# Optimization experiments

Hardware: AMD Instinct MI355X
Metric: run time of the kernel (lower is better)

The kernel has to match this reference:

```python
import jax, jax.numpy as jnp
import numpy as np

H = 32        # num heads
D = 80        # head dim
HID = 2560    # hidden size = H*D
ROT = 32      # rotary dim = int(0.4*80)
THETA = 10000.0
T = 2048      # total packed tokens
B = 4         # sequences
SEQ = 512     # tokens per sequence
CACHE = 4096  # paged cache slots


def setup_inputs() -> dict:
    key = jax.random.key(0)
    ks = jax.random.split(key, 10)
    bound = 1.0 / np.sqrt(HID)

    def lin(k):
        kw, kb = jax.random.split(k)
        W = jax.random.uniform(kw, (HID, HID), jnp.float32, -bound, bound)
        b = jax.random.uniform(kb, (HID,), jnp.float32, -bound, bound)
        return W, b

    Wq, bq = lin(ks[0])
    Wk, bk = lin(ks[1])
    Wv, bv = lin(ks[2])
    Wd, bd = lin(ks[3])
    h = jax.random.normal(ks[4], (T, HID), jnp.float32)
    return {
        "h": h,
        "k_cache": jnp.zeros((CACHE, HID), jnp.float32),
        "v_cache": jnp.zeros((CACHE, HID), jnp.float32),
        "positions": (jnp.arange(T) % SEQ).astype(jnp.int32),
        "offsets": (jnp.arange(B + 1) * SEQ).astype(jnp.int32),
        "cache_indices": jnp.arange(T, dtype=jnp.int32),
        "Wq": Wq, "bq": bq, "Wk": Wk, "bk": bk,
        "Wv": Wv, "bv": bv, "Wd": Wd, "bd": bd,
    }


def _rotate_half(x):
    x1, x2 = jnp.split(x, 2, axis=-1)
    return jnp.concatenate([-x2, x1], axis=-1)


def reference(h, k_cache, v_cache, positions, offsets, cache_indices,
              Wq, bq, Wk, bk, Wv, bv, Wd, bd):
    # QKV projections (torch Linear: x @ W.T + b)
    q = h @ Wq.T + bq
    k = h @ Wk.T + bk
    v = h @ Wv.T + bv

    q3 = q.reshape(T, H, D)
    k3 = k.reshape(T, H, D)

    # partial RoPE on first ROT dims of each head
    pos = positions.astype(jnp.float32)
    inv_freq = 1.0 / (THETA ** (jnp.arange(0, ROT, 2, dtype=jnp.float32) / ROT))
    freqs = pos[:, None] * inv_freq                      # [T, ROT/2]
    emb = jnp.concatenate([freqs, freqs], axis=-1)       # [T, ROT]
    cos = jnp.cos(emb)[:, None, :]                       # [T, 1, ROT]
    sin = jnp.sin(emb)[:, None, :]

    q_rot, q_pass = q3[..., :ROT], q3[..., ROT:]
    k_rot, k_pass = k3[..., :ROT], k3[..., ROT:]
    q_rot = q_rot * cos + _rotate_half(q_rot) * sin
    k_rot = k_rot * cos + _rotate_half(k_rot) * sin
    q3 = jnp.concatenate([q_rot, q_pass], axis=-1)
    k3 = jnp.concatenate([k_rot, k_pass], axis=-1)

    # prompt_init=True path: scatter rotated k and v into paged caches
    new_k_cache = k_cache.at[cache_indices].set(k3.reshape(T, HID))
    new_v_cache = v_cache.at[cache_indices].set(v)

    # variable-length causal attention over packed sequences
    scale = D ** -0.5
    scores = jnp.einsum('thd,shd->hts', q3, k3) * scale   # [H, T, T]
    idx = jnp.arange(T)
    seg = jnp.searchsorted(offsets[1:], idx, side='right')
    mask = (seg[:, None] == seg[None, :]) & (idx[:, None] >= idx[None, :])
    scores = jnp.where(mask[None], scores, jnp.float32(-1e30))
    p = jax.nn.softmax(scores, axis=-1)
    o = jnp.einsum('hts,shd->thd', p, v.reshape(T, H, D)).reshape(T, HID)

    out = o @ Wd.T + bd
    return out, new_k_cache, new_v_cache
```

## Files before the change

### kernel.cpp

```cpp
#include <hip/hip_runtime.h>
#include <cstdint>
#include <cstddef>


#define HIDDEN 2560
#define SEQT 2048
#define NHEADS 32
#define DHEAD 80
#define NSEG 4
#define SEGLEN 512
#define CACHE_ROWS 4096
#define QSCALE 0.11180339887498949f

typedef __bf16 bf16_8 __attribute__((ext_vector_type(8)));
typedef unsigned short u16x8 __attribute__((ext_vector_type(8)));
typedef float f32x4 __attribute__((ext_vector_type(4)));

__device__ __forceinline__ unsigned short f2bf(float f) {
  unsigned int u = __builtin_bit_cast(unsigned int, f);
  u += 0x7fffu + ((u >> 16) & 1u);
  return (unsigned short)(u >> 16);
}
__device__ __forceinline__ float bf2f(unsigned short s) {
  unsigned int u = ((unsigned int)s) << 16;
  return __builtin_bit_cast(float, u);
}

__device__ __forceinline__ void gload16(const unsigned short* g, unsigned short* l) {
  __builtin_amdgcn_global_load_lds(
      (const __attribute__((address_space(1))) unsigned int*)g,
      (__attribute__((address_space(3))) unsigned int*)l, 16, 0, 0);
}

#define BAR() asm volatile("s_barrier" ::: "memory")
#define LGKM0()                                          \
  do {                                                   \
    asm volatile("s_waitcnt lgkmcnt(0)" ::: "memory");   \
    __builtin_amdgcn_sched_barrier(0);                   \
  } while (0)
#define PRIO(x) __builtin_amdgcn_s_setprio(x)
#define MF(af, bf, c) c = __builtin_amdgcn_mfma_f32_16x16x32_bf16(af, bf, c, 0, 0, 0)

__global__ __launch_bounds__(256) void cast_kernel(
    const float* __restrict__ src, unsigned short* __restrict__ dst, int n4) {
  int i = blockIdx.x * blockDim.x + threadIdx.x;
  const int stride = gridDim.x * blockDim.x;
  for (; i < n4; i += stride) {
    float4 v = ((const float4*)src)[i];
    ushort4 o;
    o.x = f2bf(v.x); o.y = f2bf(v.y); o.z = f2bf(v.z); o.w = f2bf(v.w);
    ((ushort4*)dst)[i] = o;
  }
}

__global__ __launch_bounds__(256) void cast4_kernel(
    const float* __restrict__ s0, const float* __restrict__ s1,
    const float* __restrict__ s2, const float* __restrict__ s3,
    unsigned short* __restrict__ d0, unsigned short* __restrict__ d1,
    unsigned short* __restrict__ d2, unsigned short* __restrict__ d3, int n4) {
  const float* s = blockIdx.z == 0 ? s0 : blockIdx.z == 1 ? s1 : blockIdx.z == 2 ? s2 : s3;
  unsigned short* d = blockIdx.z == 0 ? d0 : blockIdx.z == 1 ? d1 : blockIdx.z == 2 ? d2 : d3;
  int i = blockIdx.x * blockDim.x + threadIdx.x;
  const int stride = gridDim.x * blockDim.x;
  for (; i < n4; i += stride) {
    float4 v = ((const float4*)s)[i];
    ushort4 o;
    o.x = f2bf(v.x); o.y = f2bf(v.y); o.z = f2bf(v.z); o.w = f2bf(v.w);
    ((ushort4*)d)[i] = o;
  }
}

template <int OUTMODE, int NT>
__device__ __forceinline__ void gemm256_body(
    const unsigned short* __restrict__ A, const unsigned short* __restrict__ Bg,
    const float* __restrict__ bias, void* __restrict__ C,
    int m0, int n0, int kbase) {
  constexpr int K = HIDDEN;
  static_assert((NT & 1) == 0 && NT >= 4, "NT must be even");
  __shared__ __align__(16) unsigned short L[65536];

  const int tid = threadIdx.x;
  const int lane = tid & 63;
  const int wid = tid >> 6;
  const int l15 = lane & 15;
  const int kg = lane >> 4;
  const int wm = wid >> 2;
  const int wn = wid & 3;

  const int g8 = (((tid & 7) - (tid >> 3)) & 7) * 8;
  const int srow = tid >> 3;
  const unsigned short* As0 = A + (size_t)(m0 + srow) * K + kbase + g8;
  const unsigned short* As1 = As0 + (size_t)128 * K;
  const unsigned short* Bs0 = Bg + (size_t)(n0 + srow) * K + kbase + g8;
  const unsigned short* Bs1 = Bs0 + (size_t)128 * K;
  const int t16 = tid * 8;

  auto stA0 = [&](int kt) {
    const int b = (kt & 1) * 32768, ko = kt * 64;
    gload16(As0 + ko, L + b + t16);
    gload16(As1 + ko, L + b + 8192 + t16);
  };
  auto stA1 = [&](int kt) {
    const int b = (kt & 1) * 32768, ko = 64 * K + kt * 64;
    gload16(As0 + ko, L + b + 4096 + t16);
    gload16(As1 + ko, L + b + 12288 + t16);
  };
  auto stB0 = [&](int kt) {
    const int b = (kt & 1) * 32768 + 16384, ko = kt * 64;
    gload16(Bs0 + ko, L + b + t16);
    gload16(Bs0 + 64 * K + ko, L + b + 4096 + t16);
  };
  auto stB1 = [&](int kt) {
    const int b = (kt & 1) * 32768 + 16384 + 8192, ko = kt * 64;
    gload16(Bs1 + ko, L + b + t16);
    gload16(Bs1 + 64 * K + ko, L + b + 4096 + t16);
  };

  const int c0 = (kg + l15) & 7;
  const int aof0 = wm * 8192 + l15 * 64 + c0 * 8;
  const int aof1 = wm * 8192 + l15 * 64 + (c0 ^ 4) * 8;
  const int bof0 = 16384 + wn * 4096 + l15 * 64 + c0 * 8;
  const int bof1 = 16384 + wn * 4096 + l15 * 64 + (c0 ^ 4) * 8;

  f32x4 acc[8][4];
#pragma unroll
  for (int m = 0; m < 8; m++)
#pragma unroll
    for (int n = 0; n < 4; n++) acc[m][n] = f32x4{0.f, 0.f, 0.f, 0.f};

  bf16_8 a[4][2], bl[2][2], bh[2][2];

#define DSR(off) (*(const bf16_8*)(L + (off)))
  auto rdA = [&](int off) {
#pragma unroll
    for (int fm = 0; fm < 4; fm++) {
      a[fm][0] = DSR(off + aof0 + fm * 1024);
      a[fm][1] = DSR(off + aof1 + fm * 1024);
    }
  };
  auto rdBl = [&](int off) {
#pragma unroll
    for (int fn = 0; fn < 2; fn++) {
      bl[fn][0] = DSR(off + bof0 + fn * 1024);
      bl[fn][1] = DSR(off + bof1 + fn * 1024);
    }
  };
  auto rdBh = [&](int off) {
#pragma unroll
    for (int fn = 0; fn < 2; fn++) {
      bh[fn][0] = DSR(off + bof0 + (2 + fn) * 1024);
      bh[fn][1] = DSR(off + bof1 + (2 + fn) * 1024);
    }
  };
  auto mmq = [&](int mq, int nq, bf16_8 (&bb)[2][2]) {
#pragma unroll
    for (int fm = 0; fm < 4; fm++)
#pragma unroll
      for (int fn = 0; fn < 2; fn++) {
        MF(a[fm][0], bb[fn][0], acc[mq * 4 + fm][nq * 2 + fn]);
        MF(a[fm][1], bb[fn][1], acc[mq * 4 + fm][nq * 2 + fn]);
      }
  };

  stA0(0); stB0(0); stB1(0); stA1(0);
  stA0(1); stB0(1); stB1(1);
  asm volatile("s_waitcnt vmcnt(6)" ::: "memory");
  BAR();

#pragma unroll 2
  for (int t = 0; t < NT - 2; ++t) {
    const int bo = (t & 1) * 32768;
    rdA(bo); rdBl(bo);
    stA1(t + 1);
    BAR(); LGKM0(); PRIO(1); mmq(0, 0, bl); PRIO(0); BAR();
    rdBh(bo);
    stA0(t + 2);
    BAR(); LGKM0(); PRIO(1); mmq(0, 1, bh); PRIO(0); BAR();
    rdA(bo + 4096);
    stB0(t + 2);
    BAR(); LGKM0(); PRIO(1); mmq(1, 0, bl); PRIO(0); BAR();
    stB1(t + 2);
    BAR(); PRIO(1); mmq(1, 1, bh); PRIO(0);
    asm volatile("s_waitcnt vmcnt(6)" ::: "memory");
    BAR();
  }

  {
    const int bo = 0;
    rdA(bo); rdBl(bo);
    stA1(NT - 1);
    BAR(); LGKM0(); PRIO(1); mmq(0, 0, bl); PRIO(0); BAR();
    rdBh(bo);
    BAR(); LGKM0(); PRIO(1); mmq(0, 1, bh); PRIO(0); BAR();
    rdA(bo + 4096);
    BAR(); LGKM0(); PRIO(1); mmq(1, 0, bl); PRIO(0); BAR();
    BAR(); PRIO(1); mmq(1, 1, bh); PRIO(0);
    asm volatile("s_waitcnt vmcnt(0)" ::: "memory");
    BAR();
  }
  {
    const int bo = 32768;
    rdA(bo); rdBl(bo);
    BAR(); LGKM0(); PRIO(1); mmq(0, 0, bl); PRIO(0); BAR();
    rdBh(bo);
    BAR(); LGKM0(); PRIO(1); mmq(0, 1, bh); PRIO(0); BAR();
    rdA(bo + 4096);
    BAR(); LGKM0(); PRIO(1); mmq(1, 0, bl); PRIO(0); BAR();
    PRIO(1); mmq(1, 1, bh); PRIO(0);
  }
#undef DSR

#pragma unroll
  for (int n4 = 0; n4 < 4; n4++) {
    const int col = n0 + wn * 64 + n4 * 16 + l15;
    const float bv = (OUTMODE == 2) ? 0.f : bias[col];
#pragma unroll
    for (int m8 = 0; m8 < 8; m8++) {
      const int rowb = m0 + wm * 128 + m8 * 16 + kg * 4;
#pragma unroll
      for (int j = 0; j < 4; j++) {
        float val = acc[m8][n4][j] + bv;
        if (OUTMODE == 0)
          ((unsigned short*)C)[(size_t)(rowb + j) * HIDDEN + col] = f2bf(val);
        else
          ((float*)C)[(size_t)(rowb + j) * HIDDEN + col] = val;
      }
    }
  }
}

__global__ __launch_bounds__(512, 2) void gemm_qkv8_kernel(
    const unsigned short* __restrict__ A,
    const unsigned short* __restrict__ B0, const unsigned short* __restrict__ B1,
    const unsigned short* __restrict__ B2,
    const float* __restrict__ bias0, const float* __restrict__ bias1,
    const float* __restrict__ bias2,
    unsigned short* __restrict__ C0, unsigned short* __restrict__ C1,
    unsigned short* __restrict__ C2) {
  const int lb = blockIdx.x + 8 * (blockIdx.y + 10 * blockIdx.z);
  const int swz = (lb & 7) * 30 + (lb >> 3);
  const int mx = swz & 7;
  const int r = swz >> 3;
  const int ny = r % 10;
  const int zz = r / 10;
  const unsigned short* B = zz == 0 ? B0 : (zz == 1 ? B1 : B2);
  const float* bias = zz == 0 ? bias0 : (zz == 1 ? bias1 : bias2);
  unsigned short* C = zz == 0 ? C0 : (zz == 1 ? C1 : C2);
  gemm256_body<0, 40>(A, B, bias, C, mx * 256, ny * 256, 0);
}

__global__ __launch_bounds__(512, 2) void gemm_out8_kernel(
    const unsigned short* __restrict__ A, const unsigned short* __restrict__ B,
    float* __restrict__ P0, float* __restrict__ P1) {
  const int lb = blockIdx.x + 8 * (blockIdx.y + 10 * blockIdx.z);
  const int swz = (lb & 7) * 20 + (lb >> 3);
  const int mx = swz & 7;
  const int r = swz >> 3;
  const int ny = r % 10;
  const int kz = r / 10;
  float* P = kz == 0 ? P0 : P1;
  gemm256_body<2, 20>(A, B, nullptr, P, mx * 256, ny * 256, kz * 1280);
}

__global__ __launch_bounds__(256) void reduce_bias_kernel(
    const float* __restrict__ p0, const float* __restrict__ p1,
    const float* __restrict__ bias, float* __restrict__ out, int n4) {
  int i = blockIdx.x * blockDim.x + threadIdx.x;
  const int stride = gridDim.x * blockDim.x;
  for (; i < n4; i += stride) {
    float4 a = ((const float4*)p0)[i];
    float4 b = ((const float4*)p1)[i];
    const int cb = (i * 4) % HIDDEN;
    float4 bv = *(const float4*)&bias[cb];
    float4 o;
    o.x = a.x + b.x + bv.x;
    o.y = a.y + b.y + bv.y;
    o.z = a.z + b.z + bv.z;
    o.w = a.w + b.w + bv.w;
    ((float4*)out)[i] = o;
  }
}

__global__ __launch_bounds__(256) void rope_scatter_kernel(
    unsigned short* __restrict__ qb, unsigned short* __restrict__ kb,
    const unsigned short* __restrict__ vb,
    const int* __restrict__ positions, const int* __restrict__ cidx,
    float* __restrict__ kco, float* __restrict__ vco) {
  const int t = blockIdx.x;
  const int tid = threadIdx.x;
  __shared__ float cs[16], sn[16];

  if (tid < 16) {
    const float pos = (float)positions[t];
    const float inv = expf(-(float)tid * (9.210340371976184f / 16.0f));
    const float f = pos * inv;
    cs[tid] = cosf(f);
    sn[tid] = sinf(f);
  }
  __syncthreads();

  for (int i = tid; i < 1024; i += 256) {
    const int which = i >> 9;
    const int p = i & 511;
    const int hh = p >> 4, d = p & 15;
    unsigned short* buf = which ? kb : qb;
    const size_t base = (size_t)t * HIDDEN + hh * DHEAD + d;
    const float x1 = bf2f(buf[base]);
    const float x2 = bf2f(buf[base + 16]);
    const float c = cs[d], s = sn[d];
    buf[base] = f2bf(x1 * c - x2 * s);
    buf[base + 16] = f2bf(x2 * c + x1 * s);
  }
  __syncthreads();

  const int ci = cidx[t];
  float* krow = kco + (size_t)ci * HIDDEN;
  float* vrow = vco + (size_t)ci * HIDDEN;
  const unsigned short* ks = kb + (size_t)t * HIDDEN;
  const unsigned short* vs = vb + (size_t)t * HIDDEN;
  for (int i = tid; i < HIDDEN; i += 256) {
    krow[i] = bf2f(ks[i]);
    vrow[i] = bf2f(vs[i]);
  }
}

#define KSTR 104
#define VSTR 72
#define PSTR 72

__global__ __launch_bounds__(256) void attn_mfma_kernel(
    const unsigned short* __restrict__ qb, const unsigned short* __restrict__ kb,
    const unsigned short* __restrict__ vb, unsigned short* __restrict__ ob) {
  const int qt = blockIdx.x;
  const int h = blockIdx.y;
  const int seg = blockIdx.z;
  const int tq0 = seg * SEGLEN + qt * 64;

  __shared__ unsigned short Kt[64 * KSTR];
  __shared__ unsigned short VtT[80 * VSTR];
  __shared__ unsigned short Pw[4][16 * PSTR];

  const int tid = threadIdx.x;
  const int lane = tid & 63;
  const int w = tid >> 6;
  const int l15 = lane & 15;
  const int g = lane >> 4;

  bf16_8 qa[3];
  {
    const unsigned short* qp = qb + (size_t)(tq0 + w * 16 + l15) * HIDDEN + h * DHEAD;
#pragma unroll
    for (int c = 0; c < 3; c++) {
      u16x8 t = (u16x8)(unsigned short)0;
      const int d0 = c * 32 + g * 8;
      if (d0 < DHEAD) {
#pragma unroll
        for (int e = 0; e < 8; e++) t[e] = f2bf(bf2f(qp[d0 + e]) * QSCALE);
      }
      qa[c] = __builtin_bit_cast(bf16_8, t);
    }
  }

  float m_[4], l_[4];
#pragma unroll
  for (int j = 0; j < 4; j++) { m_[j] = -3.0e38f; l_[j] = 0.f; }
  f32x4 Oacc[5];
#pragma unroll
  for (int n = 0; n < 5; n++) Oacc[n] = f32x4{0.f, 0.f, 0.f, 0.f};

  for (int st = 0; st <= qt; ++st) {
    const int ts0 = seg * SEGLEN + st * 64;
    __syncthreads();
    for (int i = tid; i < 64 * 20; i += 256) {
      const int row = i / 20;
      const int c = i - row * 20;
      const size_t gsrc = (size_t)(ts0 + row) * HIDDEN + h * DHEAD + c * 4;
      ushort4 kv = *(const ushort4*)(kb + gsrc);
      ushort4 vv = *(const ushort4*)(vb + gsrc);
      *(ushort4*)&Kt[row * KSTR + c * 4] = kv;
      VtT[(c * 4 + 0) * VSTR + row] = vv.x;
      VtT[(c * 4 + 1) * VSTR + row] = vv.y;
      VtT[(c * 4 + 2) * VSTR + row] = vv.z;
      VtT[(c * 4 + 3) * VSTR + row] = vv.w;
    }
    __syncthreads();

    f32x4 Sacc[4];
#pragma unroll
    for (int t = 0; t < 4; t++) Sacc[t] = f32x4{0.f, 0.f, 0.f, 0.f};
#pragma unroll
    for (int c = 0; c < 3; c++) {
#pragma unroll
      for (int t = 0; t < 4; t++) {
        bf16_8 kf;
        if (c < 2 || g < 2)
          kf = *(const bf16_8*)&Kt[(t * 16 + l15) * KSTR + c * 32 + g * 8];
        else
          kf = __builtin_bit_cast(bf16_8, (u16x8)(unsigned short)0);
        Sacc[t] = __builtin_amdgcn_mfma_f32_16x16x32_bf16(qa[c], kf, Sacc[t], 0, 0, 0);
      }
    }

    if (st == qt) {
#pragma unroll
      for (int t = 0; t < 4; t++)
#pragma unroll
        for (int j = 0; j < 4; j++)
          if (t * 16 + l15 > w * 16 + 4 * g + j) Sacc[t][j] = -1e30f;
    }

    float pm[4], ps[4], rold[4];
#pragma unroll
    for (int j = 0; j < 4; j++)
      pm[j] = fmaxf(fmaxf(Sacc[0][j], Sacc[1][j]), fmaxf(Sacc[2][j], Sacc[3][j]));
#pragma unroll
    for (int d = 1; d < 16; d <<= 1)
#pragma unroll
      for (int j = 0; j < 4; j++) pm[j] = fmaxf(pm[j], __shfl_xor(pm[j], d, 64));
#pragma unroll
    for (int j = 0; j < 4; j++) {
      const float mn = fmaxf(m_[j], pm[j]);
      rold[j] = __expf(m_[j] - mn);
      m_[j] = mn;
      ps[j] = 0.f;
    }
#pragma unroll
    for (int t = 0; t < 4; t++)
#pragma unroll
      for (int j = 0; j < 4; j++) {
        const float p = __expf(Sacc[t][j] - m_[j]);
        Sacc[t][j] = p;
        ps[j] += p;
      }
#pragma unroll
    for (int d = 1; d < 16; d <<= 1)
#pragma unroll
      for (int j = 0; j < 4; j++) ps[j] += __shfl_xor(ps[j], d, 64);
#pragma unroll
    for (int j = 0; j < 4; j++) l_[j] = l_[j] * rold[j] + ps[j];

#pragma unroll
    for (int t = 0; t < 4; t++)
#pragma unroll
      for (int j = 0; j < 4; j++)
        Pw[w][(4 * g + j) * PSTR + t * 16 + l15] = f2bf(Sacc[t][j]);
#pragma unroll
    for (int n = 0; n < 5; n++)
#pragma unroll
      for (int j = 0; j < 4; j++) Oacc[n][j] *= rold[j];

#pragma unroll
    for (int c = 0; c < 2; c++) {
      bf16_8 pa = *(const bf16_8*)&Pw[w][l15 * PSTR + c * 32 + g * 8];
#pragma unroll
      for (int n = 0; n < 5; n++) {
        bf16_8 vf = *(const bf16_8*)&VtT[(n * 16 + l15) * VSTR + c * 32 + g * 8];
        Oacc[n] = __builtin_amdgcn_mfma_f32_16x16x32_bf16(pa, vf, Oacc[n], 0, 0, 0);
      }
    }
  }

  float inv[4];
#pragma unroll
  for (int j = 0; j < 4; j++) inv[j] = 1.f / l_[j];
  unsigned short* op = ob + (size_t)(tq0 + w * 16) * HIDDEN + h * DHEAD;
#pragma unroll
  for (int n = 0; n < 5; n++)
#pragma unroll
    for (int j = 0; j < 4; j++)
      op[(size_t)(4 * g + j) * HIDDEN + n * 16 + l15] = f2bf(Oacc[n][j] * inv[j]);
}

extern "C" void kernel_launch(void* const* d_in, const int* in_sizes, int n_in,
                              void* d_out, int out_size, void* d_ws, size_t ws_size,
                              hipStream_t stream) {
  const float* h = (const float*)d_in[0];
  const float* kci = (const float*)d_in[1];
  const float* vci = (const float*)d_in[2];
  const int* positions = (const int*)d_in[3];
  const int* cidx = (const int*)d_in[5];
  const float* Wq = (const float*)d_in[6];
  const float* bq = (const float*)d_in[7];
  const float* Wk = (const float*)d_in[8];
  const float* bk = (const float*)d_in[9];
  const float* Wv = (const float*)d_in[10];
  const float* bv = (const float*)d_in[11];
  const float* Wd = (const float*)d_in[12];
  const float* bd = (const float*)d_in[13];

  float* out = (float*)d_out;
  float* kco = out + (size_t)SEQT * HIDDEN;
  float* vco = kco + (size_t)CACHE_ROWS * HIDDEN;

  char* ws = (char*)d_ws;
  char* ws0 = ws;
  unsigned short* h_bf = (unsigned short*)ws;  ws += (size_t)SEQT * HIDDEN * 2;
  unsigned short* Wq_bf = (unsigned short*)ws; ws += (size_t)HIDDEN * HIDDEN * 2;
  unsigned short* Wk_bf = (unsigned short*)ws; ws += (size_t)HIDDEN * HIDDEN * 2;
  unsigned short* Wv_bf = (unsigned short*)ws; ws += (size_t)HIDDEN * HIDDEN * 2;
  unsigned short* Wd_bf = (unsigned short*)ws; ws += (size_t)HIDDEN * HIDDEN * 2;
  unsigned short* q_bf = (unsigned short*)ws;  ws += (size_t)SEQT * HIDDEN * 2;
  unsigned short* k_bf = (unsigned short*)ws;  ws += (size_t)SEQT * HIDDEN * 2;
  unsigned short* v_bf = (unsigned short*)ws;  ws += (size_t)SEQT * HIDDEN * 2;
  unsigned short* o_bf = (unsigned short*)ws;  ws += (size_t)SEQT * HIDDEN * 2;

  float* part0 = (float*)ws0;
  float* part1 = part0 + (size_t)SEQT * HIDDEN;

  const size_t half = (size_t)SEQT * HIDDEN;
  hipMemcpyAsync(kco + half, kci + half, half * 4, hipMemcpyDeviceToDevice, stream);
  hipMemcpyAsync(vco + half, vci + half, half * 4, hipMemcpyDeviceToDevice, stream);

  cast_kernel<<<2048, 256, 0, stream>>>(h, h_bf, SEQT * HIDDEN / 4);
  {
    dim3 gc(2048, 1, 4);
    cast4_kernel<<<gc, 256, 0, stream>>>(Wq, Wk, Wv, Wd, Wq_bf, Wk_bf, Wv_bf, Wd_bf,
                                         HIDDEN * HIDDEN / 4);
  }

  {
    dim3 gq(SEQT / 256, HIDDEN / 256, 3);
    gemm_qkv8_kernel<<<gq, 512, 0, stream>>>(h_bf, Wq_bf, Wk_bf, Wv_bf, bq, bk, bv,
                                             q_bf, k_bf, v_bf);
  }

  rope_scatter_kernel<<<SEQT, 256, 0, stream>>>(q_bf, k_bf, v_bf, positions, cidx, kco, vco);

  {
    dim3 ga(SEGLEN / 64, NHEADS, NSEG);
    attn_mfma_kernel<<<ga, 256, 0, stream>>>(q_bf, k_bf, v_bf, o_bf);
  }

  {
    dim3 go(SEQT / 256, HIDDEN / 256, 2);
    gemm_out8_kernel<<<go, 512, 0, stream>>>(o_bf, Wd_bf, part0, part1);
  }
  reduce_bias_kernel<<<2048, 256, 0, stream>>>(part0, part1, bd, out,
                                               SEQT * HIDDEN / 4);
}
```

Before: 259.4 us.

## Use three-way split-K for output GEMM and merge cast/copy launches

```diff
diff --git a/kernel.cpp b/kernel.cpp
--- a/kernel.cpp
+++ b/kernel.cpp
@@ -41,25 +41,17 @@
 #define PRIO(x) __builtin_amdgcn_s_setprio(x)
 #define MF(af, bf, c) c = __builtin_amdgcn_mfma_f32_16x16x32_bf16(af, bf, c, 0, 0, 0)
 
-__global__ __launch_bounds__(256) void cast_kernel(
-    const float* __restrict__ src, unsigned short* __restrict__ dst, int n4) {
-  int i = blockIdx.x * blockDim.x + threadIdx.x;
-  const int stride = gridDim.x * blockDim.x;
-  for (; i < n4; i += stride) {
-    float4 v = ((const float4*)src)[i];
-    ushort4 o;
-    o.x = f2bf(v.x); o.y = f2bf(v.y); o.z = f2bf(v.z); o.w = f2bf(v.w);
-    ((ushort4*)dst)[i] = o;
-  }
-}
-
-__global__ __launch_bounds__(256) void cast4_kernel(
+__global__ __launch_bounds__(256) void cast5_kernel(
     const float* __restrict__ s0, const float* __restrict__ s1,
     const float* __restrict__ s2, const float* __restrict__ s3,
+    const float* __restrict__ s4,
     unsigned short* __restrict__ d0, unsigned short* __restrict__ d1,
-    unsigned short* __restrict__ d2, unsigned short* __restrict__ d3, int n4) {
-  const float* s = blockIdx.z == 0 ? s0 : blockIdx.z == 1 ? s1 : blockIdx.z == 2 ? s2 : s3;
-  unsigned short* d = blockIdx.z == 0 ? d0 : blockIdx.z == 1 ? d1 : blockIdx.z == 2 ? d2 : d3;
+    unsigned short* __restrict__ d2, unsigned short* __restrict__ d3,
+    unsigned short* __restrict__ d4) {
+  const int z = blockIdx.z;
+  const float* s = z == 0 ? s0 : z == 1 ? s1 : z == 2 ? s2 : z == 3 ? s3 : s4;
+  unsigned short* d = z == 0 ? d0 : z == 1 ? d1 : z == 2 ? d2 : z == 3 ? d3 : d4;
+  const int n4 = (z < 4) ? (HIDDEN * HIDDEN / 4) : (SEQT * HIDDEN / 4);
   int i = blockIdx.x * blockDim.x + threadIdx.x;
   const int stride = gridDim.x * blockDim.x;
   for (; i < n4; i += stride) {
@@ -70,13 +62,27 @@
   }
 }
 
-template <int OUTMODE, int NT>
+__global__ __launch_bounds__(256) void copy_upper_kernel(
+    const float* __restrict__ kci, const float* __restrict__ vci,
+    float* __restrict__ kco, float* __restrict__ vco) {
+  const int n4half = SEQT * HIDDEN / 4;
+  int i = blockIdx.x * blockDim.x + threadIdx.x;
+  const int stride = gridDim.x * blockDim.x;
+  for (; i < 2 * n4half; i += stride) {
+    const int w = i >= n4half;
+    const int j = i - w * n4half + n4half;
+    const float4* s = w ? (const float4*)vci : (const float4*)kci;
+    float4* d = w ? (float4*)vco : (float4*)kco;
+    d[j] = s[j];
+  }
+}
+
+template <int OUTMODE>
 __device__ __forceinline__ void gemm256_body(
     const unsigned short* __restrict__ A, const unsigned short* __restrict__ Bg,
     const float* __restrict__ bias, void* __restrict__ C,
-    int m0, int n0, int kbase) {
+    int m0, int n0, int kbase, int nt) {
   constexpr int K = HIDDEN;
-  static_assert((NT & 1) == 0 && NT >= 4, "NT must be even");
   __shared__ __align__(16) unsigned short L[65536];
 
   const int tid = threadIdx.x;
@@ -168,7 +174,7 @@
   BAR();
 
 #pragma unroll 2
-  for (int t = 0; t < NT - 2; ++t) {
+  for (int t = 0; t < nt - 2; ++t) {
     const int bo = (t & 1) * 32768;
     rdA(bo); rdBl(bo);
     stA1(t + 1);
@@ -188,7 +194,7 @@
   {
     const int bo = 0;
     rdA(bo); rdBl(bo);
-    stA1(NT - 1);
+    stA1(nt - 1);
     BAR(); LGKM0(); PRIO(1); mmq(0, 0, bl); PRIO(0); BAR();
     rdBh(bo);
     BAR(); LGKM0(); PRIO(1); mmq(0, 1, bh); PRIO(0); BAR();
@@ -246,37 +252,41 @@
   const unsigned short* B = zz == 0 ? B0 : (zz == 1 ? B1 : B2);
   const float* bias = zz == 0 ? bias0 : (zz == 1 ? bias1 : bias2);
   unsigned short* C = zz == 0 ? C0 : (zz == 1 ? C1 : C2);
-  gemm256_body<0, 40>(A, B, bias, C, mx * 256, ny * 256, 0);
+  gemm256_body<0>(A, B, bias, C, mx * 256, ny * 256, 0, 40);
 }
 
 __global__ __launch_bounds__(512, 2) void gemm_out8_kernel(
     const unsigned short* __restrict__ A, const unsigned short* __restrict__ B,
-    float* __restrict__ P0, float* __restrict__ P1) {
+    float* __restrict__ P0, float* __restrict__ P1, float* __restrict__ P2) {
   const int lb = blockIdx.x + 8 * (blockIdx.y + 10 * blockIdx.z);
-  const int swz = (lb & 7) * 20 + (lb >> 3);
+  const int swz = (lb & 7) * 30 + (lb >> 3);
   const int mx = swz & 7;
   const int r = swz >> 3;
   const int ny = r % 10;
   const int kz = r / 10;
-  float* P = kz == 0 ? P0 : P1;
-  gemm256_body<2, 20>(A, B, nullptr, P, mx * 256, ny * 256, kz * 1280);
-}
-
-__global__ __launch_bounds__(256) void reduce_bias_kernel(
+  float* P = kz == 0 ? P0 : (kz == 1 ? P1 : P2);
+  const int kbase = kz * 896;
+  const int nt = (kz == 2) ? 12 : 14;
+  gemm256_body<2>(A, B, nullptr, P, mx * 256, ny * 256, kbase, nt);
+}
+
+__global__ __launch_bounds__(256) void reduce3_bias_kernel(
     const float* __restrict__ p0, const float* __restrict__ p1,
-    const float* __restrict__ bias, float* __restrict__ out, int n4) {
+    const float* __restrict__ p2, const float* __restrict__ bias,
+    float* __restrict__ out, int n4) {
   int i = blockIdx.x * blockDim.x + threadIdx.x;
   const int stride = gridDim.x * blockDim.x;
   for (; i < n4; i += stride) {
     float4 a = ((const float4*)p0)[i];
     float4 b = ((const float4*)p1)[i];
+    float4 c = ((const float4*)p2)[i];
     const int cb = (i * 4) % HIDDEN;
     float4 bv = *(const float4*)&bias[cb];
     float4 o;
-    o.x = a.x + b.x + bv.x;
-    o.y = a.y + b.y + bv.y;
-    o.z = a.z + b.z + bv.z;
-    o.w = a.w + b.w + bv.w;
+    o.x = a.x + b.x + c.x + bv.x;
+    o.y = a.y + b.y + c.y + bv.y;
+    o.z = a.z + b.z + c.z + bv.z;
+    o.w = a.w + b.w + c.w + bv.w;
     ((float4*)out)[i] = o;
   }
 }
@@ -506,16 +516,14 @@
 
   float* part0 = (float*)ws0;
   float* part1 = part0 + (size_t)SEQT * HIDDEN;
-
-  const size_t half = (size_t)SEQT * HIDDEN;
-  hipMemcpyAsync(kco + half, kci + half, half * 4, hipMemcpyDeviceToDevice, stream);
-  hipMemcpyAsync(vco + half, vci + half, half * 4, hipMemcpyDeviceToDevice, stream);
-
-  cast_kernel<<<2048, 256, 0, stream>>>(h, h_bf, SEQT * HIDDEN / 4);
-  {
-    dim3 gc(2048, 1, 4);
-    cast4_kernel<<<gc, 256, 0, stream>>>(Wq, Wk, Wv, Wd, Wq_bf, Wk_bf, Wv_bf, Wd_bf,
-                                         HIDDEN * HIDDEN / 4);
+  float* part2 = (float*)q_bf;
+
+  copy_upper_kernel<<<2048, 256, 0, stream>>>(kci, vci, kco, vco);
+
+  {
+    dim3 gc(2048, 1, 5);
+    cast5_kernel<<<gc, 256, 0, stream>>>(Wq, Wk, Wv, Wd, h,
+                                         Wq_bf, Wk_bf, Wv_bf, Wd_bf, h_bf);
   }
 
   {
@@ -532,9 +540,9 @@
   }
 
   {
-    dim3 go(SEQT / 256, HIDDEN / 256, 2);
-    gemm_out8_kernel<<<go, 512, 0, stream>>>(o_bf, Wd_bf, part0, part1);
-  }
-  reduce_bias_kernel<<<2048, 256, 0, stream>>>(part0, part1, bd, out,
-                                               SEQT * HIDDEN / 4);
-}
+    dim3 go(SEQT / 256, HIDDEN / 256, 3);
+    gemm_out8_kernel<<<go, 512, 0, stream>>>(o_bf, Wd_bf, part0, part1, part2);
+  }
+  reduce3_bias_kernel<<<2048, 256, 0, stream>>>(part0, part1, part2, bd, out,
+                                                SEQT * HIDDEN / 4);
+}
```

After: 249.9 us. 3.7% less time.
